# Kernel optimization log

Measured on AMD Instinct MI355X. Metric: run time of the kernel, lower is better.

The kernel has to match this reference:

```python
import jax, jax.numpy as jnp
import numpy as np

B, H, S, DK, DV = 2, 48, 2048, 128, 128
EPS = 1e-6

def _l2norm(x):
    n = jnp.linalg.norm(x, axis=-1, keepdims=True)
    return x / jnp.maximum(n, EPS)

def setup_inputs() -> dict:
    root = jax.random.key(0)
    k0, k1, k2, k3, k4 = jax.random.split(root, 5)
    query = jax.random.normal(k0, (B, H, S, DK), jnp.float32)
    key = jax.random.normal(k1, (B, H, S, DK), jnp.float32)
    value = jax.random.normal(k2, (B, H, S, DV), jnp.float32)
    # g is a per-token log decay: negative, in (-0.5, 0)
    g = -0.5 * jax.random.uniform(k3, (B, H, S), jnp.float32)
    # beta is a sigmoid-like mixing gate in (0, 1)
    beta = jax.random.uniform(k4, (B, H, S), jnp.float32)
    return {"query": query, "key": key, "value": value, "g": g, "beta": beta}

def reference(query, key, value, g, beta):
    """Gated delta-rule linear-attention recurrence.

    state_t = state_{t-1} * exp(g_t)
    delta_t = (v_t - k_t^T state_t) * beta_t
    state_t = state_t + k_t delta_t^T
    out_t   = q_t^T state_t
    with q, k L2-normalized and q scaled by 1/sqrt(dk).
    Returns (output [B,H,S,DV], final_state [B,H,DK,DV]).
    """
    dk = query.shape[-1]
    scale = 1.0 / np.sqrt(dk).astype(np.float32)
    q = _l2norm(query) * scale
    k = _l2norm(key)
    # move seq axis to front for scan: (S, B, H, d)
    qs = jnp.moveaxis(q, 2, 0)
    ks = jnp.moveaxis(k, 2, 0)
    vs = jnp.moveaxis(value, 2, 0)
    gs = jnp.moveaxis(g, 2, 0)
    bs = jnp.moveaxis(beta, 2, 0)

    def step(state, xs):
        q_t, k_t, v_t, g_t, b_t = xs
        state = state * jnp.exp(g_t)[..., None, None]          # [B,H,DK,DV]
        kv_mem = jnp.einsum('bhk,bhkv->bhv', k_t, state)       # read
        delta = (v_t - kv_mem) * b_t[..., None]                # beta-scaled delta
        state = state + jnp.einsum('bhk,bhv->bhkv', k_t, delta)
        out = jnp.einsum('bhk,bhkv->bhv', q_t, state)
        return state, out

    init = jnp.zeros((query.shape[0], query.shape[1], dk, value.shape[-1]), query.dtype)
    final_state, outs = jax.lax.scan(step, init, (qs, ks, vs, gs, bs))
    output = jnp.moveaxis(outs, 0, 2)  # [B,H,S,DV]
    return output, final_state
```

## Files before the change

kernel.cpp:

```cpp
#include <hip/hip_runtime.h>

typedef __attribute__((ext_vector_type(8)))  short short8;
typedef __attribute__((ext_vector_type(4)))  float f32x4;
typedef __attribute__((ext_vector_type(16))) float f32x16;
typedef __attribute__((ext_vector_type(4)))  unsigned short ushort4v;

#define NH   96
#define SEQL 2048
#define DD   128
#define CC   64
#define NCH  32
#define SK   136
#define S64  72
#define SLOT 4608

__device__ __forceinline__ unsigned short f2bf(float f){
  union { float f; unsigned u; } v; v.f = f;
  unsigned r = v.u + 0x7FFFu + ((v.u >> 16) & 1u);
  return (unsigned short)(r >> 16);
}
__device__ __forceinline__ float bf2f(unsigned short u){
  union { unsigned u; float f; } v; v.u = ((unsigned)u) << 16; return v.f;
}
__device__ __forceinline__ short8 frg(const unsigned short* b, int stride, int row0, int kt, int lane){
  return *(const short8*)&b[(row0 + (lane & 31)) * stride + (kt << 4) + ((lane >> 5) << 3)];
}
__device__ __forceinline__ short8 ifrag(int n0, int kt, int lane){
  const int idx = n0 + (lane & 31) - (kt << 4) - ((lane >> 5) << 3);
  short8 v;
  #pragma unroll
  for (int e = 0; e < 8; ++e) v[e] = (short)((e == idx) ? 0x3F80 : 0);
  return v;
}
#define MM32(A,B,C) __builtin_amdgcn_mfma_f32_32x32x16_bf16(A,B,C,0,0,0)
__device__ __forceinline__ f32x16 z16(){
  return (f32x16){0.f,0.f,0.f,0.f,0.f,0.f,0.f,0.f,0.f,0.f,0.f,0.f,0.f,0.f,0.f,0.f};
}
template<int KTN>
__device__ __forceinline__ f32x16 gemm32(const unsigned short* A, int sa, int m0,
                                         const unsigned short* B, int sb, int n0,
                                         f32x16 acc, int lane){
  #pragma unroll
  for (int kt = 0; kt < KTN; ++kt)
    acc = MM32(frg(A, sa, m0, kt, lane), frg(B, sb, n0, kt, lane), acc);
  return acc;
}
__device__ __forceinline__ void stq(unsigned short* buf, int stride, int n0, int m0, int lane, f32x16 v){
  const int nn = n0 + (lane & 31), hh = (lane >> 5) << 2;
  #pragma unroll
  for (int q = 0; q < 4; ++q) {
    ushort4v pv;
    #pragma unroll
    for (int s = 0; s < 4; ++s) pv[s] = f2bf(v[4*q + s]);
    *(ushort4v*)&buf[nn * stride + m0 + 8*q + hh] = pv;
  }
}
__device__ __forceinline__ f32x16 ldq(const unsigned short* buf, int stride, int n0, int m0, int lane){
  f32x16 a;
  const int nn = n0 + (lane & 31), hh = (lane >> 5) << 2;
  #pragma unroll
  for (int q = 0; q < 4; ++q) {
    ushort4v pv = *(const ushort4v*)&buf[nn * stride + m0 + 8*q + hh];
    #pragma unroll
    for (int s = 0; s < 4; ++s) a[4*q + s] = bf2f(pv[s]);
  }
  return a;
}
__device__ __forceinline__ f32x16 pinit(const unsigned short* lo, const unsigned short* hi,
                                        int nt, int m0, int lane){
  const unsigned short* base = (nt ? hi : lo) + (lane & 31) * S64;
  const int hh = (lane >> 5) << 2;
  f32x16 p;
  #pragma unroll
  for (int q = 0; q < 4; ++q) {
    ushort4v t = *(const ushort4v*)&base[m0 + 8*q + hh];
    #pragma unroll
    for (int s = 0; s < 4; ++s) p[4*q + s] = bf2f(t[s]);
  }
  return p;
}
#define BAR() do { asm volatile("s_waitcnt lgkmcnt(0)" ::: "memory"); __builtin_amdgcn_s_barrier(); } while(0)

#define REC  36864
#define QOFF 0
#define WOFF 8192
#define UOFF 16384
#define KOFF 24576
#define MOFF 32768

#define AOF 0
#define BOF 9216
#define XS0 17920
#define XS1 22528
#define XS2 27136
#define XS3 31744
#define MRO 36352

__global__ __launch_bounds__(512, 4)
void gdn_prep(const float* __restrict__ Qg, const float* __restrict__ Kg,
              const float* __restrict__ Vg, const float* __restrict__ Gg,
              const float* __restrict__ Bg,
              unsigned short* __restrict__ wsp, float* __restrict__ wcs)
{
  __shared__ unsigned short a[40448];
  __shared__ float s_swv[64], s_swiv[64], s_sbe[64];

  const int tid = threadIdx.x, w = tid >> 6, lane = tid & 63;
  const int mt = (w & 3) >> 1, nt = w & 1;
  const int hc = blockIdx.x, head = hc >> 5, c = hc & 31;
  const int t0 = c * CC;
  const size_t rb = (size_t)head * SEQL * DD + (size_t)t0 * DD;
  const float* kp = Kg + rb;
  const float* qp = Qg + rb;
  const float* vp = Vg + rb;
  const float* gp = Gg + (size_t)head * SEQL + t0;
  const float* bp = Bg + (size_t)head * SEQL + t0;
  unsigned short* rec = wsp + (size_t)hc * REC;

  const int lrow = tid >> 3;
  const int c16  = (tid & 7) * 16;
  const int c8p  = (tid & 7) * 8;

  f32x4 kr[4], qr[4];
  #pragma unroll
  for (int i = 0; i < 4; ++i) {
    kr[i] = *(const f32x4*)(kp + (size_t)lrow * DD + c16 + 4*i);
    qr[i] = *(const f32x4*)(qp + (size_t)lrow * DD + c16 + 4*i);
  }
  float gl = gp[lane], bl = bp[lane];
  float sc = gl;
  #pragma unroll
  for (int d = 1; d < 64; d <<= 1) { float t = __shfl_up(sc, d); if (lane >= d) sc += t; }
  float wv = __expf(sc);
  if (w == 0) { s_swv[lane] = wv; s_swiv[lane] = __expf(-sc); s_sbe[lane] = bl; }
  float ssk = 0.f, ssq = 0.f;
  #pragma unroll
  for (int i = 0; i < 4; ++i) {
    ssk += kr[i][0]*kr[i][0] + kr[i][1]*kr[i][1] + kr[i][2]*kr[i][2] + kr[i][3]*kr[i][3];
    ssq += qr[i][0]*qr[i][0] + qr[i][1]*qr[i][1] + qr[i][2]*qr[i][2] + qr[i][3]*qr[i][3];
  }
  ssk += __shfl_xor(ssk, 1); ssk += __shfl_xor(ssk, 2); ssk += __shfl_xor(ssk, 4);
  ssq += __shfl_xor(ssq, 1); ssq += __shfl_xor(ssq, 2); ssq += __shfl_xor(ssq, 4);
  const float ik = 1.f / fmaxf(sqrtf(ssk), 1e-6f);
  const float wl = __shfl(wv, lrow);
  const float iq = 0.08838834764831845f / fmaxf(sqrtf(ssq), 1e-6f) * wl;
  #pragma unroll
  for (int i = 0; i < 4; ++i) {
    ushort4v pk, pq;
    #pragma unroll
    for (int r = 0; r < 4; ++r) { pk[r] = f2bf(kr[i][r]*ik); pq[r] = f2bf(qr[i][r]*iq); }
    *(ushort4v*)&a[AOF + lrow*SK + c16 + 4*i] = pk;
    *(ushort4v*)&a[BOF + lrow*SK + c16 + 4*i] = pq;
    *(ushort4v*)(rec + QOFF + lrow*DD + c16 + 4*i) = pq;
  }
  BAR();

  if (w < 4) {
    f32x16 ckk = gemm32<8>(a+AOF, SK, 32*mt, a+AOF, SK, 32*nt, z16(), lane);
    const int nn = 32*nt + (lane & 31), hh = (lane >> 5) << 2;
    const float ben = s_sbe[nn], wvn = s_swv[nn], sin = s_swiv[nn];
    #pragma unroll
    for (int q = 0; q < 4; ++q) {
      ushort4v xT, xR;
      #pragma unroll
      for (int si = 0; si < 4; ++si) {
        const int r = 4*q + si, mm = 32*mt + 8*q + hh + si;
        const float svm = s_swv[mm], sim = s_swiv[mm], bem = s_sbe[mm];
        xT[si] = (mm > nn) ? f2bf(bem*svm*sin*ckk[r]) : 0;
        xR[si] = (nn > mm) ? f2bf(ben*wvn*sim*ckk[r]) : 0;
      }
      const int off = nn*S64 + 32*mt + 8*q + hh;
      *(ushort4v*)&a[XS1 + off] = xT;
      *(ushort4v*)&a[XS0 + off] = xR;
    }
  } else {
    f32x16 ckq = gemm32<8>(a+AOF, SK, 32*mt, a+BOF, SK, 32*nt, z16(), lane);
    const int nn = 32*nt + (lane & 31), hh = (lane >> 5) << 2;
    #pragma unroll
    for (int q = 0; q < 4; ++q) {
      ushort4v mv;
      #pragma unroll
      for (int si = 0; si < 4; ++si) {
        const int r = 4*q + si, mm = 32*mt + 8*q + hh + si;
        mv[si] = (mm <= nn) ? f2bf(ckq[r]*s_swiv[mm]) : 0;
      }
      *(ushort4v*)(rec + MOFF + nn*64 + 32*mt + 8*q + hh) = mv;
    }
  }
  BAR();

  f32x4 vr[4];
  #pragma unroll
  for (int i = 0; i < 4; ++i)
    vr[i] = *(const f32x4*)(vp + (size_t)lrow * DD + c16 + 4*i);
  if (w < 4) {
    f32x16 c1 = gemm32<4>(a+XS0, S64, 32*mt, a+XS1, S64, 32*nt, z16(), lane);
    stq(a+XS3, S64, 32*nt, 32*mt, lane, c1);
  } else {
    f32x16 c2 = gemm32<4>(a+XS1, S64, 32*mt, a+XS0, S64, 32*nt, z16(), lane);
    stq(a+XS2, S64, 32*nt, 32*mt, lane, c2);
  }
  {
    unsigned short* p0 = a + ((lrow < 32) ? BOF : BOF+2304) + (lrow & 31)*S64;
    const unsigned short* x0 = a + XS0 + lrow*S64;
    short8 xv = *(const short8*)&x0[c8p];
    short8 ov;
    #pragma unroll
    for (int e = 0; e < 8; ++e) {
      const int col = c8p + e;
      ov[e] = (short)f2bf(((col == lrow) ? 1.f : 0.f) - bf2f((unsigned short)xv[e]));
    }
    *(short8*)&p0[c8p] = ov;
  }
  BAR();

  if (w < 4) {
    f32x16 c1 = gemm32<4>(a+XS2, S64, 32*mt, a+XS3, S64, 32*nt, z16(), lane);
    stq(a+XS1, S64, 32*nt, 32*mt, lane, c1);
    f32x16 p = pinit(a+BOF, a+BOF+2304, nt, 32*mt, lane);
    p = gemm32<4>(a+XS3, S64, 32*mt, (nt ? a+BOF+2304 : a+BOF), S64, 0, p, lane);
    stq((nt ? a+MRO : a+BOF+SLOT), S64, 0, 32*mt, lane, p);
  } else {
    f32x16 c2 = gemm32<4>(a+XS3, S64, 32*mt, a+XS2, S64, 32*nt, z16(), lane);
    stq(a+XS0, S64, 32*nt, 32*mt, lane, c2);
  }
  BAR();

  if (w < 4) {
    f32x16 c1 = gemm32<4>(a+XS0, S64, 32*mt, a+XS1, S64, 32*nt, z16(), lane);
    stq(a+XS2, S64, 32*nt, 32*mt, lane, c1);
  } else {
    f32x16 p = pinit(a+BOF+SLOT, a+MRO, nt, 32*mt, lane);
    p = gemm32<4>(a+XS1, S64, 32*mt, (nt ? a+MRO : a+BOF+SLOT), S64, 0, p, lane);
    stq((nt ? a+BOF+2304 : a+BOF), S64, 0, 32*mt, lane, p);
  }
  BAR();

  if (w < 4) {
    f32x16 p = pinit(a+BOF, a+BOF+2304, nt, 32*mt, lane);
    p = gemm32<4>(a+XS2, S64, 32*mt, (nt ? a+BOF+2304 : a+BOF), S64, 0, p, lane);
    stq((nt ? a+MRO : a+BOF+SLOT), S64, 0, 32*mt, lane, p);
  }
  #pragma unroll
  for (int i = 0; i < 4; ++i)
    #pragma unroll
    for (int r = 0; r < 4; ++r)
      a[XS0 + (c16 + 4*i + r)*S64 + lrow] = f2bf(vr[i][r]);
  BAR();

  {
    unsigned short* trow  = a + ((lrow < 32) ? BOF+SLOT : MRO) + (lrow & 31)*S64;
    unsigned short* t3row = a + ((lrow < 32) ? BOF : BOF+2304) + (lrow & 31)*S64;
    short8 tv = *(const short8*)&trow[c8p];
    short8 o2, o3;
    #pragma unroll
    for (int e = 0; e < 8; ++e) {
      const int j = c8p + e;
      const float t = bf2f((unsigned short)tv[e]);
      o2[e] = (short)f2bf(-t * s_sbe[j] * s_swv[j]);
      o3[e] = (short)f2bf( t * s_sbe[j]);
    }
    *(short8*)&trow[c8p]  = o2;
    *(short8*)&t3row[c8p] = o3;
  }
  {
    const int j = w >> 2, d4 = w & 3;
    const float wcv = s_swv[63];
    f32x16 ckt = z16();
    #pragma unroll
    for (int kk = 0; kk < 2; ++kk) {
      const int kt = 2*d4 + kk;
      ckt = MM32(frg(a+AOF, SK, 32*j, kt, lane), ifrag(32*d4, kt, lane), ckt);
    }
    stq(a+XS2, S64, 32*d4, 32*j, lane, ckt);
    const int nn = 32*d4 + (lane & 31), hh = (lane >> 5) << 2;
    #pragma unroll
    for (int q = 0; q < 4; ++q) {
      ushort4v o;
      #pragma unroll
      for (int si = 0; si < 4; ++si) {
        const int tok = 32*j + 8*q + hh + si;
        o[si] = f2bf(ckt[4*q+si] * wcv * s_swiv[tok]);
      }
      *(ushort4v*)(rec + KOFF + nn*64 + 32*j + 8*q + hh) = o;
    }
  }
  BAR();

  {
    const int j = w >> 2, d4 = w & 3;
    const int nn = lane & 31, hh = (lane >> 5) << 2;
    f32x16 cw = gemm32<4>(a+XS2, S64, 32*d4, (j ? a+MRO : a+BOF+SLOT), S64, 0, z16(), lane);
    #pragma unroll
    for (int q = 0; q < 4; ++q) {
      ushort4v pw;
      #pragma unroll
      for (int si = 0; si < 4; ++si) pw[si] = f2bf(cw[4*q+si]);
      *(ushort4v*)(rec + WOFF + (32*j + nn)*128 + 32*d4 + 8*q + hh) = pw;
    }
    f32x16 cu = gemm32<4>((j ? a+BOF+2304 : a+BOF), S64, 0, a+XS0, S64, 32*d4, z16(), lane);
    #pragma unroll
    for (int q = 0; q < 4; ++q) {
      ushort4v pu;
      #pragma unroll
      for (int si = 0; si < 4; ++si) pu[si] = f2bf(cu[4*q+si]);
      *(ushort4v*)(rec + UOFF + (32*d4 + nn)*64 + 32*j + 8*q + hh) = pu;
    }
    if (tid == 0) wcs[hc] = s_swv[63];
  }
}

#define SU   72
#define OW0  0
#define OW1  8704
#define OK0  17408
#define OK1  26624
#define OU0  35840
#define OU1  40448
#define OM0  45056
#define OM1  49664
#define OS0  54272
#define OS1  62976
#define ODT  71680

__global__ __launch_bounds__(512, 1)
void gdn_scan(const unsigned short* __restrict__ wsp, const float* __restrict__ wcs,
              float* __restrict__ Out, float* __restrict__ FS)
{
  __shared__ unsigned short a[76288];

  const int tid = threadIdx.x, w = tid >> 6, lane = tid & 63;
  const int head = blockIdx.x % NH, vh = blockIdx.x / NH;
  const unsigned short* recs = wsp + (size_t)head * NCH * REC;
  const float* wcsh = wcs + head * NCH;
  float* op = Out + (size_t)head * SEQL * DD + vh * 64;

  const int mtS = w >> 1, ntS = w & 1;
  const bool outw = (w < 4);

  f32x16 s = z16();

  const int wr = tid >> 3, wc16 = (tid & 7) * 16;
  const int kr = tid >> 2, kc16 = (tid & 3) * 16;
  const int ur = tid >> 3, uc8 = (tid & 7) * 8;

  short8 stW0, stW1, stK0, stK1, stU, stM, qb[8];
  float wcn = 0.f;

  auto issue = [&](int c){
    const unsigned short* rec = recs + (size_t)c * REC;
    stW0 = *(const short8*)(rec + WOFF + wr*128 + wc16);
    stW1 = *(const short8*)(rec + WOFF + wr*128 + wc16 + 8);
    stK0 = *(const short8*)(rec + KOFF + kr*64 + kc16);
    stK1 = *(const short8*)(rec + KOFF + kr*64 + kc16 + 8);
    stU  = *(const short8*)(rec + UOFF + (vh*64 + ur)*64 + uc8);
    stM  = *(const short8*)(rec + MOFF + ur*64 + uc8);
    if (outw) {
      #pragma unroll
      for (int kt = 0; kt < 8; ++kt)
        qb[kt] = *(const short8*)(rec + QOFF + (32*mtS + (lane & 31))*DD + kt*16 + ((lane >> 5) << 3));
    }
    wcn = wcsh[c];
  };
  auto dswrite = [&](int par){
    unsigned short* bw = a + (par ? OW1 : OW0);
    *(short8*)&bw[wr*SK + wc16]     = stW0;
    *(short8*)&bw[wr*SK + wc16 + 8] = stW1;
    unsigned short* bk = a + (par ? OK1 : OK0);
    *(short8*)&bk[kr*SU + kc16]     = stK0;
    *(short8*)&bk[kr*SU + kc16 + 8] = stK1;
    unsigned short* bu = a + (par ? OU1 : OU0);
    *(short8*)&bu[ur*SU + uc8] = stU;
    unsigned short* bm = a + (par ? OM1 : OM0);
    *(short8*)&bm[ur*SU + uc8] = stM;
  };

  issue(0);
  float wc_cur = wcn;
  dswrite(0);
  stq(a+OS0, SK, 32*ntS, 32*mtS, lane, s);
  BAR();

  for (int c = 0; c < NCH; ++c) {
    const int cur = c & 1;
    const unsigned short* W_ = a + (cur ? OW1 : OW0);
    const unsigned short* K_ = a + (cur ? OK1 : OK0);
    const unsigned short* U_ = a + (cur ? OU1 : OU0);
    const unsigned short* M_ = a + (cur ? OM1 : OM0);
    const unsigned short* S_ = a + (cur ? OS1 : OS0);
    unsigned short* Sn       = a + (cur ? OS0 : OS1);

    f32x16 oq = z16();
    if (outw) {
      #pragma unroll
      for (int kt = 0; kt < 8; ++kt)
        oq = MM32(qb[kt], frg(S_, SK, 32*ntS, kt, lane), oq);
    }
    if (c < NCH-1) issue(c+1);

    {
      f32x16 d0 = gemm32<8>(W_, SK, 0,  S_, SK, 32*ntS, z16(), lane);
      f32x16 d1 = gemm32<8>(W_, SK, 32, S_, SK, 32*ntS, z16(), lane);
      const int nn = 32*ntS + (lane & 31), hh = (lane >> 5) << 2;
      #pragma unroll
      for (int q = 0; q < 4; ++q) {
        ushort4v u0 = *(const ushort4v*)&U_[nn*SU + 0  + 8*q + hh];
        ushort4v u1 = *(const ushort4v*)&U_[nn*SU + 32 + 8*q + hh];
        ushort4v p0, p1;
        #pragma unroll
        for (int si = 0; si < 4; ++si) {
          p0[si] = f2bf(d0[4*q+si] + bf2f(u0[si]));
          p1[si] = f2bf(d1[4*q+si] + bf2f(u1[si]));
        }
        *(ushort4v*)&a[ODT + nn*SU + 0  + 8*q + hh] = p0;
        *(ushort4v*)&a[ODT + nn*SU + 32 + 8*q + hh] = p1;
      }
    }

    {
      f32x16 sa;
      #pragma unroll
      for (int r = 0; r < 16; ++r) sa[r] = s[r] * wc_cur;
      s = gemm32<4>(K_, SU, 32*mtS, a+ODT, SU, 32*ntS, sa, lane);
    }

    if (outw) {
      f32x16 o = gemm32<4>(M_, SU, 32*mtS, a+ODT, SU, 32*ntS, oq, lane);
      const int vv = 32*ntS + (lane & 31), hh = (lane >> 5) << 2;
      float* ob = op + (size_t)(c*CC + 32*mtS) * DD + vv;
      #pragma unroll
      for (int q = 0; q < 4; ++q)
        #pragma unroll
        for (int si = 0; si < 4; ++si)
          ob[(size_t)(si + 8*q + hh) * DD] = o[4*q + si];
    }

    stq(Sn, SK, 32*ntS, 32*mtS, lane, s);
    if (c < NCH-1) dswrite(cur ^ 1);
    wc_cur = wcn;
    BAR();
  }

  {
    float* fsp = FS + (size_t)head * DD * DD + vh * 64;
    const int nn = 32*ntS + (lane & 31), hh = (lane >> 5) << 2;
    #pragma unroll
    for (int q = 0; q < 4; ++q)
      #pragma unroll
      for (int si = 0; si < 4; ++si)
        fsp[(size_t)(32*mtS + si + 8*q + hh) * DD + nn] = s[4*q + si];
  }
}

__global__ __launch_bounds__(512, 1)
void gdn_chunk2(const float* __restrict__ Qg, const float* __restrict__ Kg,
                const float* __restrict__ Vg, const float* __restrict__ Gg,
                const float* __restrict__ Bg,
                float* __restrict__ Out, float* __restrict__ FS)
{
  __shared__ __align__(16) unsigned short sKc[64*SK];
  __shared__ __align__(16) unsigned short sQc[64*SK];
  __shared__ __align__(16) unsigned short sS0T[64*SK];
  __shared__ __align__(16) unsigned short sVc[64*S64];
  __shared__ __align__(16) unsigned short sVT[64*S64];
  __shared__ __align__(16) unsigned short sM[64*S64];
  __shared__ __align__(16) unsigned short sAr[8*SLOT];
  __shared__ float sbe2[2][64], swv2[2][64], swiv2[2][64];

  const int tid  = threadIdx.x;
  const int w    = tid >> 6;
  const int lane = tid & 63;
  const int half = w >> 2;
  const int j    = w & 3;
  const int mt   = j >> 1, nt = j & 1;
  const int mtS  = w >> 1, ntS = w & 1;
  const int mtK  = w >> 2, ntK = w & 3;
  const int head = blockIdx.x % NH;
  const int vh   = blockIdx.x / NH;

  const size_t rb = (size_t)head * SEQL * DD;
  const float* qp = Qg + rb;
  const float* kp = Kg + rb;
  const float* vp = Vg + rb + vh * 64;
  const float* gp = Gg + (size_t)head * SEQL;
  const float* bp = Bg + (size_t)head * SEQL;
  float* op  = Out + rb + vh * 64;
  float* fsp = FS + (size_t)head * DD * DD + vh * 64;

  const int lrow = tid >> 3;
  const int c16  = (tid & 7) * 16;
  const int c8   = (tid & 7) * 8;

  unsigned short* const sl0 = sAr + 0*SLOT;
  unsigned short* const sl1 = sAr + 1*SLOT;
  unsigned short* const sl2 = sAr + 2*SLOT;
  unsigned short* const sl3 = sAr + 3*SLOT;
  unsigned short* const sl4 = sAr + 4*SLOT;
  unsigned short* const sl5 = sAr + 5*SLOT;
  unsigned short* const sl6 = sAr + 6*SLOT;
  unsigned short* const sl7 = sAr + 7*SLOT;

  f32x16 s = z16(), oacc = z16();
  f32x4 kr[4], qr[4], vr[2]; float gr = 0.f, br = 0.f;

  auto prefetch = [&](int t0p){
    const float* kb = kp + (size_t)(t0p + lrow) * DD + c16;
    const float* qb = qp + (size_t)(t0p + lrow) * DD + c16;
    const float* vb = vp + (size_t)(t0p + lrow) * DD + c8;
    #pragma unroll
    for (int i = 0; i < 4; ++i) { kr[i] = *(const f32x4*)(kb + 4*i); qr[i] = *(const f32x4*)(qb + 4*i); }
    #pragma unroll
    for (int i = 0; i < 2; ++i) vr[i] = *(const f32x4*)(vb + 4*i);
    if (w == 7) { gr = gp[t0p + lane]; br = bp[t0p + lane]; }
  };
  auto scan_to = [&](int p){
    if (w == 7) {
      float sc = gr;
      #pragma unroll
      for (int d = 1; d < 64; d <<= 1) { float t = __shfl_up(sc, d); if (lane >= d) sc += t; }
      swv2[p][lane]  = __expf(sc);
      swiv2[p][lane] = __expf(-sc);
      sbe2[p][lane]  = br;
    }
  };

  prefetch(0);
  scan_to(0);
  BAR();

  for (int tc = 0; tc < NCH; ++tc) {
    const int t0 = tc * CC;
    const int cur = tc & 1, nxt = cur ^ 1;
    {
      float ssk = 0.f, ssq = 0.f;
      #pragma unroll
      for (int i = 0; i < 4; ++i) {
        ssk += kr[i][0]*kr[i][0] + kr[i][1]*kr[i][1] + kr[i][2]*kr[i][2] + kr[i][3]*kr[i][3];
        ssq += qr[i][0]*qr[i][0] + qr[i][1]*qr[i][1] + qr[i][2]*qr[i][2] + qr[i][3]*qr[i][3];
      }
      ssk += __shfl_xor(ssk, 1); ssk += __shfl_xor(ssk, 2); ssk += __shfl_xor(ssk, 4);
      ssq += __shfl_xor(ssq, 1); ssq += __shfl_xor(ssq, 2); ssq += __shfl_xor(ssq, 4);
      const float ik = 1.f / fmaxf(sqrtf(ssk), 1e-6f);
      const float iq = 0.08838834764831845f / fmaxf(sqrtf(ssq), 1e-6f) * swv2[cur][lrow];
      #pragma unroll
      for (int i = 0; i < 4; ++i) {
        ushort4v pk, pq;
        #pragma unroll
        for (int r = 0; r < 4; ++r) { pk[r] = f2bf(kr[i][r] * ik); pq[r] = f2bf(qr[i][r] * iq); }
        *(ushort4v*)&sKc[lrow*SK + c16 + 4*i] = pk;
        *(ushort4v*)&sQc[lrow*SK + c16 + 4*i] = pq;
      }
      #pragma unroll
      for (int i = 0; i < 2; ++i) {
        ushort4v pv;
        #pragma unroll
        for (int r = 0; r < 4; ++r) pv[r] = f2bf(vr[i][r]);
        *(ushort4v*)&sVc[lrow*S64 + c8 + 4*i] = pv;
      }
    }
    stq(sS0T, SK, 32*ntS, 32*mtS, lane, s);
    prefetch(tc < NCH-1 ? (tc+1)*CC : t0);
    BAR();

    if (half == 0) {
      f32x16 aa = gemm32<8>(sKc, SK, 32*mt, sKc, SK, 32*nt, z16(), lane);
      const int nn = 32*nt + (lane & 31), hh = (lane >> 5) << 2;
      #pragma unroll
      for (int q = 0; q < 4; ++q) {
        ushort4v pR, pL, pPT, pP;
        #pragma unroll
        for (int si = 0; si < 4; ++si) {
          const int r = 4*q + si, mm = 32*mt + 8*q + hh + si;
          const float S = aa[r];
          const float av  = (mm > nn) ? sbe2[cur][mm]*swv2[cur][mm]*swiv2[cur][nn]*S : 0.f;
          const float atr = (nn > mm) ? sbe2[cur][nn]*swv2[cur][nn]*swiv2[cur][mm]*S : 0.f;
          pR[si]  = f2bf(av);
          pL[si]  = f2bf(atr);
          pPT[si] = f2bf(((mm==nn)?1.f:0.f) - av);
          pP[si]  = f2bf(((mm==nn)?1.f:0.f) - atr);
        }
        const int off = nn*S64 + 32*mt + 8*q + hh;
        *(ushort4v*)&sl1[off] = pR;
        *(ushort4v*)&sl0[off] = pL;
        *(ushort4v*)&sl5[off] = pPT;
        *(ushort4v*)&sl4[off] = pP;
      }
    } else {
      f32x16 aa = gemm32<8>(sKc, SK, 32*mt, sQc, SK, 32*nt, z16(), lane);
      const int nn = 32*nt + (lane & 31), hh = (lane >> 5) << 2;
      #pragma unroll
      for (int q = 0; q < 4; ++q) {
        ushort4v pv;
        #pragma unroll
        for (int si = 0; si < 4; ++si) {
          const int r = 4*q + si, mm = 32*mt + 8*q + hh + si;
          pv[si] = f2bf((mm <= nn) ? aa[r]*swiv2[cur][mm] : 0.f);
        }
        *(ushort4v*)&sM[nn*S64 + 32*mt + 8*q + hh] = pv;
      }
    }
    BAR();

    if (half == 0) {
      f32x16 aa = gemm32<4>(sl0, S64, 32*mt, sl1, S64, 32*nt, z16(), lane);
      stq(sl3, S64, 32*nt, 32*mt, lane, aa);
      f32x16 bb = z16();
      #pragma unroll
      for (int kk = 0; kk < 2; ++kk) {
        const int kt = 2*nt + kk;
        bb = MM32(frg(sVc, S64, 32*mt, kt, lane), ifrag(32*nt, kt, lane), bb);
      }
      stq(sVT, S64, 32*nt, 32*mt, lane, bb);
    } else {
      f32x16 aa = gemm32<4>(sl1, S64, 32*mt, sl0, S64, 32*nt, z16(), lane);
      stq(sl2, S64, 32*nt, 32*mt, lane, aa);
      oacc = gemm32<8>(sQc, SK, 32*mt, sS0T, SK, 32*nt, z16(), lane);
    }
    BAR();

    {
      unsigned short* const inL[3]   = { sl2, sl0, sl2 };
      unsigned short* const inR[3]   = { sl3, sl1, sl3 };
      unsigned short* const outL[3]  = { sl0, sl2, sl0 };
      unsigned short* const outR[3]  = { sl1, sl3, sl1 };
      unsigned short* const inP[3]   = { sl4, sl7, sl5 };
      unsigned short* const inPT[3]  = { sl5, sl6, sl4 };
      unsigned short* const outP[3]  = { sl7, sl5, sl7 };
      unsigned short* const outPT[3] = { sl6, sl4, sl6 };
      #pragma unroll
      for (int lev = 0; lev < 3; ++lev) {
        if (half == 0) {
          f32x16 aa = gemm32<4>(inL[lev], S64, 32*mt, inR[lev], S64, 32*nt, z16(), lane);
          stq(outR[lev], S64, 32*nt, 32*mt, lane, aa);
          f32x16 p = ldq(inPT[lev], S64, 32*nt, 32*mt, lane);
          p = gemm32<4>(inP[lev], S64, 32*mt, inR[lev], S64, 32*nt, p, lane);
          stq(outPT[lev], S64, 32*nt, 32*mt, lane, p);
        } else {
          f32x16 aa = gemm32<4>(inR[lev], S64, 32*mt, inL[lev], S64, 32*nt, z16(), lane);
          stq(outL[lev], S64, 32*nt, 32*mt, lane, aa);
          f32x16 p = ldq(inP[lev], S64, 32*nt, 32*mt, lane);
          p = gemm32<4>(inR[lev], S64, 32*mt, inP[lev], S64, 32*nt, p, lane);
          stq(outP[lev], S64, 32*nt, 32*mt, lane, p);
        }
        BAR();
      }
    }

    if (half == 0) {
      f32x16 aa = gemm32<4>(sl0, S64, 32*mt, sl1, S64, 32*nt, z16(), lane);
      stq(sl2, S64, 32*nt, 32*mt, lane, aa);
    } else {
      f32x16 p = ldq(sl7, S64, 32*nt, 32*mt, lane);
      p = gemm32<4>(sl1, S64, 32*mt, sl7, S64, 32*nt, p, lane);
      stq(sl4, S64, 32*nt, 32*mt, lane, p);
    }
    BAR();

    if (half == 0) {
      f32x16 p = ldq(sl4, S64, 32*nt, 32*mt, lane);
      p = gemm32<4>(sl2, S64, 32*mt, sl4, S64, 32*nt, p, lane);
      const int nn = 32*nt + (lane & 31), hh = (lane >> 5) << 2;
      #pragma unroll
      for (int q = 0; q < 4; ++q) {
        ushort4v p2, p3;
        #pragma unroll
        for (int si = 0; si < 4; ++si) {
          const int r = 4*q + si, mm = 32*mt + 8*q + hh + si;
          const float t = p[r];
          p2[si] = f2bf(-t * sbe2[cur][mm] * swv2[cur][mm]);
          p3[si] = f2bf( t * sbe2[cur][mm]);
        }
        const int off = nn*S64 + 32*mt + 8*q + hh;
        *(ushort4v*)&sl1[off] = p2;
        *(ushort4v*)&sl5[off] = p3;
      }
    } else {
      f32x16 zz = gemm32<8>(sKc, SK, 32*mt, sS0T, SK, 32*nt, z16(), lane);
      stq(sl0, S64, 32*nt, 32*mt, lane, zz);
    }
    {
      f32x16 aa = z16();
      #pragma unroll
      for (int kk = 0; kk < 2; ++kk) {
        const int kt = 2*ntK + kk;
        aa = MM32(frg(sKc, SK, 32*mtK, kt, lane), ifrag(32*ntK, kt, lane), aa);
      }
      stq(sl6, S64, 32*ntK, 32*mtK, lane, aa);
    }
    BAR();

    if (half == 0) {
      f32x16 d = gemm32<4>(sl5, S64, 32*mt, sVT, S64, 32*nt, z16(), lane);
      d = gemm32<4>(sl1, S64, 32*mt, sl0, S64, 32*nt, d, lane);
      const int nn = 32*nt + (lane & 31), hh = (lane >> 5) << 2;
      const float w63 = swv2[cur][63];
      #pragma unroll
      for (int q = 0; q < 4; ++q) {
        ushort4v pt, ps;
        #pragma unroll
        for (int si = 0; si < 4; ++si) {
          const int r = 4*q + si, mm = 32*mt + 8*q + hh + si;
          pt[si] = f2bf(d[r]);
          ps[si] = f2bf(d[r] * w63 * swiv2[cur][mm]);
        }
        const int off = nn*S64 + 32*mt + 8*q + hh;
        *(ushort4v*)&sl3[off] = pt;
        *(ushort4v*)&sl2[off] = ps;
      }
    }
    scan_to(nxt);
    {
      const float w63 = swv2[cur][63];
      #pragma unroll
      for (int r = 0; r < 16; ++r) s[r] *= w63;
    }
    BAR();

    s = gemm32<4>(sl6, S64, 32*mtS, sl2, S64, 32*ntS, s, lane);
    if (half == 1) {
      f32x16 o = oacc;
      o = gemm32<4>(sM, S64, 32*mt, sl3, S64, 32*nt, o, lane);
      const int nn = 32*nt + (lane & 31), hh = (lane >> 5) << 2;
      #pragma unroll
      for (int q = 0; q < 4; ++q)
        #pragma unroll
        for (int si = 0; si < 4; ++si)
          op[(size_t)(t0 + 32*mt + 8*q + hh + si) * DD + nn] = o[4*q + si];
    }
    BAR();
  }

  {
    const int nn = 32*ntS + (lane & 31), hh = (lane >> 5) << 2;
    #pragma unroll
    for (int q = 0; q < 4; ++q)
      #pragma unroll
      for (int si = 0; si < 4; ++si)
        fsp[(size_t)(32*mtS + 8*q + hh + si) * DD + nn] = s[4*q + si];
  }
}

extern "C" void kernel_launch(void* const* d_in, const int* in_sizes, int n_in,
                              void* d_out, int out_size, void* d_ws, size_t ws_size,
                              hipStream_t stream) {
  const float* Q = (const float*)d_in[0];
  const float* K = (const float*)d_in[1];
  const float* V = (const float*)d_in[2];
  const float* G = (const float*)d_in[3];
  const float* B = (const float*)d_in[4];
  float* Out = (float*)d_out;
  float* FS  = Out + (size_t)NH * SEQL * DD;

  const size_t WS_NEED = (size_t)NH * NCH * REC * 2 + (size_t)NH * NCH * 4;
  if (ws_size >= WS_NEED) {
    unsigned short* wsp = (unsigned short*)d_ws;
    float* wcs = (float*)(wsp + (size_t)NH * NCH * REC);
    hipLaunchKernelGGL(gdn_prep, dim3(NH*NCH), dim3(512), 0, stream, Q, K, V, G, B, wsp, wcs);
    hipLaunchKernelGGL(gdn_scan, dim3(NH*2), dim3(512), 0, stream, wsp, wcs, Out, FS);
  } else {
    hipLaunchKernelGGL(gdn_chunk2, dim3(NH*2), dim3(512), 0, stream, Q, K, V, G, B, Out, FS);
  }
}
```

Before: 235.0 us.

## Load scan operands directly into registers and split delta/output work across warps

```diff
diff --git a/kernel.cpp b/kernel.cpp
--- a/kernel.cpp
+++ b/kernel.cpp
@@ -12,6 +12,7 @@
 #define NCH  32
 #define SK   136
 #define S64  72
+#define SU   72
 #define SLOT 4608
 
 __device__ __forceinline__ unsigned short f2bf(float f){
@@ -310,24 +311,12 @@
   }
 }
 
-#define SU   72
-#define OW0  0
-#define OW1  8704
-#define OK0  17408
-#define OK1  26624
-#define OU0  35840
-#define OU1  40448
-#define OM0  45056
-#define OM1  49664
-#define OS0  54272
-#define OS1  62976
-#define ODT  71680
-
-__global__ __launch_bounds__(512, 1)
+__global__ __launch_bounds__(512, 2)
 void gdn_scan(const unsigned short* __restrict__ wsp, const float* __restrict__ wcs,
               float* __restrict__ Out, float* __restrict__ FS)
 {
-  __shared__ unsigned short a[76288];
+  __shared__ unsigned short sS[64*SK];
+  __shared__ unsigned short sD[64*SU];
 
   const int tid = threadIdx.x, w = tid >> 6, lane = tid & 63;
   const int head = blockIdx.x % NH, vh = blockIdx.x / NH;
@@ -336,114 +325,103 @@
   float* op = Out + (size_t)head * SEQL * DD + vh * 64;
 
   const int mtS = w >> 1, ntS = w & 1;
-  const bool outw = (w < 4);
+  const bool dw = (w < 4);
+  const int th  = (w & 3) >> 1;
+  const int vc  = w & 1;
+  const int l31 = lane & 31, hi8 = (lane >> 5) << 3, hh = (lane >> 5) << 2;
 
   f32x16 s = z16();
 
-  const int wr = tid >> 3, wc16 = (tid & 7) * 16;
-  const int kr = tid >> 2, kc16 = (tid & 3) * 16;
-  const int ur = tid >> 3, uc8 = (tid & 7) * 8;
-
-  short8 stW0, stW1, stK0, stK1, stU, stM, qb[8];
-  float wcn = 0.f;
-
-  auto issue = [&](int c){
+  short8 A0[8], A1[8], B0[4], B1[4], C0[4], C1[4];
+  ushort4v U0[4], U1[4];
+  float wc0 = 0.f, wc1 = 0.f;
+
+  auto issue = [&](int c, short8* A, short8* B, short8* C, ushort4v* U, float& wvv){
     const unsigned short* rec = recs + (size_t)c * REC;
-    stW0 = *(const short8*)(rec + WOFF + wr*128 + wc16);
-    stW1 = *(const short8*)(rec + WOFF + wr*128 + wc16 + 8);
-    stK0 = *(const short8*)(rec + KOFF + kr*64 + kc16);
-    stK1 = *(const short8*)(rec + KOFF + kr*64 + kc16 + 8);
-    stU  = *(const short8*)(rec + UOFF + (vh*64 + ur)*64 + uc8);
-    stM  = *(const short8*)(rec + MOFF + ur*64 + uc8);
-    if (outw) {
+    if (dw) {
       #pragma unroll
       for (int kt = 0; kt < 8; ++kt)
-        qb[kt] = *(const short8*)(rec + QOFF + (32*mtS + (lane & 31))*DD + kt*16 + ((lane >> 5) << 3));
-    }
-    wcn = wcsh[c];
+        A[kt] = *(const short8*)(rec + WOFF + (32*th + l31)*128 + kt*16 + hi8);
+      const int vrow = vh*64 + 32*vc + l31;
+      #pragma unroll
+      for (int q = 0; q < 4; ++q)
+        U[q] = *(const ushort4v*)(rec + UOFF + vrow*64 + 32*th + 8*q + hh);
+    } else {
+      #pragma unroll
+      for (int kt = 0; kt < 8; ++kt)
+        A[kt] = *(const short8*)(rec + QOFF + (32*th + l31)*128 + kt*16 + hi8);
+      #pragma unroll
+      for (int kt = 0; kt < 4; ++kt)
+        C[kt] = *(const short8*)(rec + MOFF + (32*th + l31)*64 + kt*16 + hi8);
+    }
+    #pragma unroll
+    for (int kt = 0; kt < 4; ++kt)
+      B[kt] = *(const short8*)(rec + KOFF + (32*mtS + l31)*64 + kt*16 + hi8);
+    wvv = wcsh[c];
   };
-  auto dswrite = [&](int par){
-    unsigned short* bw = a + (par ? OW1 : OW0);
-    *(short8*)&bw[wr*SK + wc16]     = stW0;
-    *(short8*)&bw[wr*SK + wc16 + 8] = stW1;
-    unsigned short* bk = a + (par ? OK1 : OK0);
-    *(short8*)&bk[kr*SU + kc16]     = stK0;
-    *(short8*)&bk[kr*SU + kc16 + 8] = stK1;
-    unsigned short* bu = a + (par ? OU1 : OU0);
-    *(short8*)&bu[ur*SU + uc8] = stU;
-    unsigned short* bm = a + (par ? OM1 : OM0);
-    *(short8*)&bm[ur*SU + uc8] = stM;
-  };
-
-  issue(0);
-  float wc_cur = wcn;
-  dswrite(0);
-  stq(a+OS0, SK, 32*ntS, 32*mtS, lane, s);
-  BAR();
-
-  for (int c = 0; c < NCH; ++c) {
-    const int cur = c & 1;
-    const unsigned short* W_ = a + (cur ? OW1 : OW0);
-    const unsigned short* K_ = a + (cur ? OK1 : OK0);
-    const unsigned short* U_ = a + (cur ? OU1 : OU0);
-    const unsigned short* M_ = a + (cur ? OM1 : OM0);
-    const unsigned short* S_ = a + (cur ? OS1 : OS0);
-    unsigned short* Sn       = a + (cur ? OS0 : OS1);
-
+
+  auto body = [&](int c, short8* A, short8* B, short8* C, ushort4v* U, float wcv,
+                  short8* An, short8* Bn, short8* Cn, ushort4v* Un, float& wvn){
     f32x16 oq = z16();
-    if (outw) {
+    if (dw) {
+      f32x16 d = z16();
       #pragma unroll
       for (int kt = 0; kt < 8; ++kt)
-        oq = MM32(qb[kt], frg(S_, SK, 32*ntS, kt, lane), oq);
-    }
-    if (c < NCH-1) issue(c+1);
-
-    {
-      f32x16 d0 = gemm32<8>(W_, SK, 0,  S_, SK, 32*ntS, z16(), lane);
-      f32x16 d1 = gemm32<8>(W_, SK, 32, S_, SK, 32*ntS, z16(), lane);
-      const int nn = 32*ntS + (lane & 31), hh = (lane >> 5) << 2;
+        d = MM32(A[kt], frg(sS, SK, 32*vc, kt, lane), d);
+      const int nn = 32*vc + l31;
       #pragma unroll
       for (int q = 0; q < 4; ++q) {
-        ushort4v u0 = *(const ushort4v*)&U_[nn*SU + 0  + 8*q + hh];
-        ushort4v u1 = *(const ushort4v*)&U_[nn*SU + 32 + 8*q + hh];
-        ushort4v p0, p1;
-        #pragma unroll
-        for (int si = 0; si < 4; ++si) {
-          p0[si] = f2bf(d0[4*q+si] + bf2f(u0[si]));
-          p1[si] = f2bf(d1[4*q+si] + bf2f(u1[si]));
-        }
-        *(ushort4v*)&a[ODT + nn*SU + 0  + 8*q + hh] = p0;
-        *(ushort4v*)&a[ODT + nn*SU + 32 + 8*q + hh] = p1;
-      }
-    }
+        ushort4v pt;
+        #pragma unroll
+        for (int si = 0; si < 4; ++si)
+          pt[si] = f2bf(d[4*q + si] + bf2f(U[q][si]));
+        *(ushort4v*)&sD[nn*SU + 32*th + 8*q + hh] = pt;
+      }
+    } else {
+      #pragma unroll
+      for (int kt = 0; kt < 8; ++kt)
+        oq = MM32(A[kt], frg(sS, SK, 32*vc, kt, lane), oq);
+    }
+    if (c + 1 < NCH) issue(c + 1, An, Bn, Cn, Un, wvn);
+    BAR();
 
     {
       f32x16 sa;
       #pragma unroll
-      for (int r = 0; r < 16; ++r) sa[r] = s[r] * wc_cur;
-      s = gemm32<4>(K_, SU, 32*mtS, a+ODT, SU, 32*ntS, sa, lane);
-    }
-
-    if (outw) {
-      f32x16 o = gemm32<4>(M_, SU, 32*mtS, a+ODT, SU, 32*ntS, oq, lane);
-      const int vv = 32*ntS + (lane & 31), hh = (lane >> 5) << 2;
-      float* ob = op + (size_t)(c*CC + 32*mtS) * DD + vv;
+      for (int r = 0; r < 16; ++r) sa[r] = s[r] * wcv;
+      #pragma unroll
+      for (int kt = 0; kt < 4; ++kt)
+        sa = MM32(B[kt], frg(sD, SU, 32*ntS, kt, lane), sa);
+      s = sa;
+    }
+    if (!dw) {
+      f32x16 o = oq;
+      #pragma unroll
+      for (int kt = 0; kt < 4; ++kt)
+        o = MM32(C[kt], frg(sD, SU, 32*vc, kt, lane), o);
+      float* ob = op + (size_t)(c*CC + 32*th) * DD + 32*vc + l31;
       #pragma unroll
       for (int q = 0; q < 4; ++q)
         #pragma unroll
         for (int si = 0; si < 4; ++si)
           ob[(size_t)(si + 8*q + hh) * DD] = o[4*q + si];
     }
-
-    stq(Sn, SK, 32*ntS, 32*mtS, lane, s);
-    if (c < NCH-1) dswrite(cur ^ 1);
-    wc_cur = wcn;
-    BAR();
+    stq(sS, SK, 32*ntS, 32*mtS, lane, s);
+    BAR();
+  };
+
+  issue(0, A0, B0, C0, U0, wc0);
+  stq(sS, SK, 32*ntS, 32*mtS, lane, s);
+  BAR();
+
+  for (int cc = 0; cc < NCH; cc += 2) {
+    body(cc,     A0, B0, C0, U0, wc0, A1, B1, C1, U1, wc1);
+    body(cc + 1, A1, B1, C1, U1, wc1, A0, B0, C0, U0, wc0);
   }
 
   {
     float* fsp = FS + (size_t)head * DD * DD + vh * 64;
-    const int nn = 32*ntS + (lane & 31), hh = (lane >> 5) << 2;
+    const int nn = 32*ntS + l31;
     #pragma unroll
     for (int q = 0; q < 4; ++q)
       #pragma unroll
```

Measured after the change: 279.3 us. 1.19x slower.
